# Optimization experiments

Measured on AMD Instinct MI355X. Metric: run time of the kernel, lower is better.

## Reference

```python
import jax, jax.numpy as jnp
import numpy as np


def _aggregate(x, w, k, pad):
    """Involution-style per-pixel local conv.
    x: [N, C, H, W]; w: [N, heads, wc, k*k, H, W] (stride=1, dilation=1, zero pad).
    Returns [N, heads, C, H, W].
    """
    N, C, H, W = x.shape
    heads, wc = w.shape[1], w.shape[2]
    G = C // wc  # channel groups sharing the same per-pixel weights (c % wc)
    xp = jnp.pad(x, ((0, 0), (0, 0), (pad, pad), (pad, pad)))
    # unfold: [N, C, k*k, H, W] via k*k static shifted slices (no dynamic indexing)
    patches = jnp.stack(
        [xp[:, :, i:i + H, j:j + W] for i in range(k) for j in range(k)], axis=2
    )
    p = patches.reshape(N, G, wc, k * k, H, W)
    # out[n, e, g, v, h, w] = sum_k w[n, e, v, k, h, w] * p[n, g, v, k, h, w]
    out = jnp.einsum('nevkhw,ngvkhw->negvhw', w, p)
    return out.reshape(N, heads, C, H, W)


def reference(x, weight1, weight2):
    out1 = _aggregate(x, weight1, 3, 1)  # 3x3 branch, pad=1
    out2 = _aggregate(x, weight2, 5, 2)  # 5x5 branch, pad=2
    # output layout [N, 2, heads, C, H, W] matching the CUDA index arithmetic
    return jnp.stack([out1, out2], axis=1)


def setup_inputs() -> dict:
    key = jax.random.key(0)
    k1, k2, k3 = jax.random.split(key, 3)
    N, C, H, W = 4, 256, 56, 56
    heads, wc = 1, 32
    x = jax.random.normal(k1, (N, C, H, W), dtype=jnp.float32)
    weight1 = jax.random.normal(k2, (N, heads, wc, 9, H, W), dtype=jnp.float32)
    weight2 = jax.random.normal(k3, (N, heads, wc, 25, H, W), dtype=jnp.float32)
    return {"x": x, "weight1": weight1, "weight2": weight2}
```

## Files before the change

### kernel.cpp

```cpp
#include <hip/hip_runtime.h>


#define N_  4
#define C_  256
#define H_  56
#define W_  56
#define HW_ 3136
#define WC_ 32
#define G_  8
#define W2_ 28
#define HW2_ 1568

__global__ __launch_bounds__(256) void lconv_kernel(
    const float* __restrict__ x,
    const float* __restrict__ w1,
    const float* __restrict__ w2,
    float* __restrict__ out)
{
    const int gid = blockIdx.x * 256 + threadIdx.x;
    const int hw2 = gid % HW2_;
    const int nv  = gid / HW2_;
    const int v   = nv % WC_;
    const int n   = nv / WC_;
    const int h   = hw2 / W2_;
    const int wb  = (hw2 % W2_) * 2;
    const int hw  = h * W_ + wb;

    const float* w1t = w1 + (size_t)nv * 9  * HW_ + hw;
    const float* w2t = w2 + (size_t)nv * 25 * HW_ + hw;
    const float* xb  = x + ((size_t)n * C_ + v) * HW_ + hw;

    float acc1x[G_], acc1y[G_], acc2x[G_], acc2y[G_];
    #pragma unroll
    for (int g = 0; g < G_; ++g) { acc1x[g]=0.f; acc1y[g]=0.f; acc2x[g]=0.f; acc2y[g]=0.f; }

    const bool aok = (wb > 0);
    const bool cok = (wb < W_ - 2);

    #pragma unroll
    for (int di = 0; di < 5; ++di) {
        const int hh = h + di - 2;
        const bool hok = (hh >= 0) && (hh < H_);

        float2 wr2[5];
        #pragma unroll
        for (int dj = 0; dj < 5; ++dj)
            wr2[dj] = *(const float2*)(w2t + (size_t)(di * 5 + dj) * HW_);
        float2 wr1[3];
        if (di >= 1 && di <= 3) {
            #pragma unroll
            for (int dj = 0; dj < 3; ++dj)
                wr1[dj] = *(const float2*)(w1t + (size_t)((di - 1) * 3 + dj) * HW_);
        }

        const int rowoff = (di - 2) * W_;
        #pragma unroll
        for (int g = 0; g < G_; ++g) {
            const float* xr = xb + (size_t)g * WC_ * HW_ + rowoff;
            const float2 z = make_float2(0.f, 0.f);
            float2 xa = (hok && aok) ? *(const float2*)(xr - 2) : z;
            float2 xm =  hok         ? *(const float2*)(xr)     : z;
            float2 xc = (hok && cok) ? *(const float2*)(xr + 2) : z;
            const float xw[6] = {xa.x, xa.y, xm.x, xm.y, xc.x, xc.y};

            #pragma unroll
            for (int dj = 0; dj < 5; ++dj) {
                acc2x[g] += wr2[dj].x * xw[dj];
                acc2y[g] += wr2[dj].y * xw[dj + 1];
            }
            if (di >= 1 && di <= 3) {
                #pragma unroll
                for (int dj = 0; dj < 3; ++dj) {
                    acc1x[g] += wr1[dj].x * xw[dj + 1];
                    acc1y[g] += wr1[dj].y * xw[dj + 2];
                }
            }
        }
    }

    float* o1 = out + ((size_t)(n * 2 + 0) * C_ + v) * HW_ + hw;
    float* o2 = out + ((size_t)(n * 2 + 1) * C_ + v) * HW_ + hw;
    #pragma unroll
    for (int g = 0; g < G_; ++g) {
        *(float2*)(o1 + (size_t)g * WC_ * HW_) = make_float2(acc1x[g], acc1y[g]);
        *(float2*)(o2 + (size_t)g * WC_ * HW_) = make_float2(acc2x[g], acc2y[g]);
    }
}

extern "C" void kernel_launch(void* const* d_in, const int* in_sizes, int n_in,
                              void* d_out, int out_size, void* d_ws, size_t ws_size,
                              hipStream_t stream) {
    const float* x  = (const float*)d_in[0];
    const float* w1 = (const float*)d_in[1];
    const float* w2 = (const float*)d_in[2];
    float* out = (float*)d_out;

    const int total = N_ * WC_ * HW2_;
    dim3 grid(total / 256), block(256);
    hipLaunchKernelGGL(lconv_kernel, grid, block, 0, stream, x, w1, w2, out);
}
```

Baseline: 135.6 us.

## Split channel groups across threads and widen pixel tile to four

Each thread now computes 4 adjacent output pixels for 2 of the 8 channel groups instead of 2 pixels for all 8 groups, using float4 loads and stores. This cuts per-thread register use and multiplies thread count to raise occupancy and latency hiding. The trade-off is that per-pixel weights are now loaded by four different threads, one per group pair, increasing weight traffic that must be served from cache.

```diff
diff --git a/kernel.cpp b/kernel.cpp
--- a/kernel.cpp
+++ b/kernel.cpp
@@ -1,89 +1,102 @@
 #include <hip/hip_runtime.h>
 
 
-#define N_  4
-#define C_  256
-#define H_  56
-#define W_  56
-#define HW_ 3136
-#define WC_ 32
-#define G_  8
-#define W2_ 28
-#define HW2_ 1568
+#define N_   4
+#define C_   256
+#define H_   56
+#define W_   56
+#define HW_  3136
+#define WC_  32
+#define W4_  14
+#define HW4_ 784
 
-__global__ __launch_bounds__(256) void lconv_kernel(
+__global__ __launch_bounds__(256, 4) void lconv_kernel(
     const float* __restrict__ x,
     const float* __restrict__ w1,
     const float* __restrict__ w2,
     float* __restrict__ out)
 {
-    const int gid = blockIdx.x * 256 + threadIdx.x;
-    const int hw2 = gid % HW2_;
-    const int nv  = gid / HW2_;
-    const int v   = nv % WC_;
-    const int n   = nv / WC_;
-    const int h   = hw2 / W2_;
-    const int wb  = (hw2 % W2_) * 2;
-    const int hw  = h * W_ + wb;
+    const int gid  = blockIdx.x * 256 + threadIdx.x;
+    const int hw4  = gid % HW4_;
+    const int rest = gid / HW4_;
+    const int gh   = rest % 4;
+    const int v    = (rest / 4) % WC_;
+    const int n    = rest / (4 * WC_);
+    const int h    = hw4 / W4_;
+    const int w4   = (hw4 % W4_) * 4;
+    const int hw   = h * W_ + w4;
+    const int nv   = n * WC_ + v;
 
     const float* w1t = w1 + (size_t)nv * 9  * HW_ + hw;
     const float* w2t = w2 + (size_t)nv * 25 * HW_ + hw;
-    const float* xb  = x + ((size_t)n * C_ + v) * HW_ + hw;
+    const int c0 = (2 * gh) * WC_ + v;
+    const float* xb = x + ((size_t)n * C_ + c0) * HW_ + hw;
 
-    float acc1x[G_], acc1y[G_], acc2x[G_], acc2y[G_];
+    float a1[2][4], a2[2][4];
     #pragma unroll
-    for (int g = 0; g < G_; ++g) { acc1x[g]=0.f; acc1y[g]=0.f; acc2x[g]=0.f; acc2y[g]=0.f; }
+    for (int g = 0; g < 2; ++g)
+        #pragma unroll
+        for (int p = 0; p < 4; ++p) { a1[g][p] = 0.f; a2[g][p] = 0.f; }
 
-    const bool aok = (wb > 0);
-    const bool cok = (wb < W_ - 2);
+    const bool aok = (w4 > 0);
+    const bool cok = (w4 < W_ - 4);
 
     #pragma unroll
     for (int di = 0; di < 5; ++di) {
         const int hh = h + di - 2;
         const bool hok = (hh >= 0) && (hh < H_);
+        const bool inner = (di >= 1) && (di <= 3);
 
-        float2 wr2[5];
+        float wr2[5][4];
         #pragma unroll
-        for (int dj = 0; dj < 5; ++dj)
-            wr2[dj] = *(const float2*)(w2t + (size_t)(di * 5 + dj) * HW_);
-        float2 wr1[3];
-        if (di >= 1 && di <= 3) {
+        for (int dj = 0; dj < 5; ++dj) {
+            const float4 t = *(const float4*)(w2t + (size_t)(di * 5 + dj) * HW_);
+            wr2[dj][0] = t.x; wr2[dj][1] = t.y; wr2[dj][2] = t.z; wr2[dj][3] = t.w;
+        }
+        float wr1[3][4];
+        if (inner) {
             #pragma unroll
-            for (int dj = 0; dj < 3; ++dj)
-                wr1[dj] = *(const float2*)(w1t + (size_t)((di - 1) * 3 + dj) * HW_);
+            for (int dj = 0; dj < 3; ++dj) {
+                const float4 t = *(const float4*)(w1t + (size_t)((di - 1) * 3 + dj) * HW_);
+                wr1[dj][0] = t.x; wr1[dj][1] = t.y; wr1[dj][2] = t.z; wr1[dj][3] = t.w;
+            }
         }
 
         const int rowoff = (di - 2) * W_;
         #pragma unroll
-        for (int g = 0; g < G_; ++g) {
+        for (int g = 0; g < 2; ++g) {
             const float* xr = xb + (size_t)g * WC_ * HW_ + rowoff;
-            const float2 z = make_float2(0.f, 0.f);
-            float2 xa = (hok && aok) ? *(const float2*)(xr - 2) : z;
-            float2 xm =  hok         ? *(const float2*)(xr)     : z;
-            float2 xc = (hok && cok) ? *(const float2*)(xr + 2) : z;
-            const float xw[6] = {xa.x, xa.y, xm.x, xm.y, xc.x, xc.y};
+            const float4 z = make_float4(0.f, 0.f, 0.f, 0.f);
+            const float4 xa = (hok && aok) ? *(const float4*)(xr - 4) : z;
+            const float4 xm =  hok         ? *(const float4*)(xr)     : z;
+            const float4 xc = (hok && cok) ? *(const float4*)(xr + 4) : z;
+            const float xw[12] = {xa.x, xa.y, xa.z, xa.w,
+                                  xm.x, xm.y, xm.z, xm.w,
+                                  xc.x, xc.y, xc.z, xc.w};
 
             #pragma unroll
-            for (int dj = 0; dj < 5; ++dj) {
-                acc2x[g] += wr2[dj].x * xw[dj];
-                acc2y[g] += wr2[dj].y * xw[dj + 1];
-            }
-            if (di >= 1 && di <= 3) {
+            for (int dj = 0; dj < 5; ++dj)
                 #pragma unroll
-                for (int dj = 0; dj < 3; ++dj) {
-                    acc1x[g] += wr1[dj].x * xw[dj + 1];
-                    acc1y[g] += wr1[dj].y * xw[dj + 2];
-                }
+                for (int p = 0; p < 4; ++p)
+                    a2[g][p] += wr2[dj][p] * xw[p + dj + 2];
+            if (inner) {
+                #pragma unroll
+                for (int dj = 0; dj < 3; ++dj)
+                    #pragma unroll
+                    for (int p = 0; p < 4; ++p)
+                        a1[g][p] += wr1[dj][p] * xw[p + dj + 3];
             }
         }
     }
 
-    float* o1 = out + ((size_t)(n * 2 + 0) * C_ + v) * HW_ + hw;
-    float* o2 = out + ((size_t)(n * 2 + 1) * C_ + v) * HW_ + hw;
+    float* o1 = out + ((size_t)(n * 2 + 0) * C_ + c0) * HW_ + hw;
+    float* o2 = out + ((size_t)(n * 2 + 1) * C_ + c0) * HW_ + hw;
     #pragma unroll
-    for (int g = 0; g < G_; ++g) {
-        *(float2*)(o1 + (size_t)g * WC_ * HW_) = make_float2(acc1x[g], acc1y[g]);
-        *(float2*)(o2 + (size_t)g * WC_ * HW_) = make_float2(acc2x[g], acc2y[g]);
+    for (int g = 0; g < 2; ++g) {
+        *(float4*)(o1 + (size_t)g * WC_ * HW_) =
+            make_float4(a1[g][0], a1[g][1], a1[g][2], a1[g][3]);
+        *(float4*)(o2 + (size_t)g * WC_ * HW_) =
+            make_float4(a2[g][0], a2[g][1], a2[g][2], a2[g][3]);
     }
 }
 
@@ -95,7 +108,7 @@
     const float* w2 = (const float*)d_in[2];
     float* out = (float*)d_out;
 
-    const int total = N_ * WC_ * HW2_;
+    const int total = N_ * WC_ * 4 * HW4_;
     dim3 grid(total / 256), block(256);
     hipLaunchKernelGGL(lconv_kernel, grid, block, 0, stream, x, w1, w2, out);
 }
```

After: 252.3 us. +86.1%, slower.

## Split channel groups across four threads to raise thread-level parallelism

Applied to the files above, without the earlier changes.

Each thread now computes 2 of the 8 channel groups instead of all 8, and the grid grows fourfold. Groups are interleaved into the low bits of the thread index, so four neighbouring lanes share the same per-pixel weights. The goal is higher occupancy and more latency hiding on a kernel that launched only a few blocks per CU. The trade-offs are redundant weight loads, x loads strided across channels within a wavefront, an un-unrolled di loop, and always-executed 3x3 FMAs on zeroed weights in the outer rows.

```diff
diff --git a/kernel.cpp b/kernel.cpp
--- a/kernel.cpp
+++ b/kernel.cpp
@@ -1,14 +1,13 @@
 #include <hip/hip_runtime.h>
 
 
-#define N_  4
-#define C_  256
-#define H_  56
-#define W_  56
-#define HW_ 3136
-#define WC_ 32
-#define G_  8
-#define W2_ 28
+#define N_   4
+#define C_   256
+#define H_   56
+#define W_   56
+#define HW_  3136
+#define WC_  32
+#define W2_  28
 #define HW2_ 1568
 
 __global__ __launch_bounds__(256) void lconv_kernel(
@@ -18,36 +17,42 @@
     float* __restrict__ out)
 {
     const int gid = blockIdx.x * 256 + threadIdx.x;
-    const int hw2 = gid % HW2_;
-    const int nv  = gid / HW2_;
-    const int v   = nv % WC_;
-    const int n   = nv / WC_;
+    const int gh  = gid & 3;
+    const int t   = gid >> 2;
+    const int hw2 = t % HW2_;
+    const int nv  = t / HW2_;
+    const int v   = nv & 31;
+    const int n   = nv >> 5;
     const int h   = hw2 / W2_;
     const int wb  = (hw2 % W2_) * 2;
     const int hw  = h * W_ + wb;
 
     const float* w1t = w1 + (size_t)nv * 9  * HW_ + hw;
     const float* w2t = w2 + (size_t)nv * 25 * HW_ + hw;
-    const float* xb  = x + ((size_t)n * C_ + v) * HW_ + hw;
+    const int c0 = gh * 64 + v;
+    const float* xb = x + ((size_t)n * C_ + c0) * HW_ + hw;
 
-    float acc1x[G_], acc1y[G_], acc2x[G_], acc2y[G_];
-    #pragma unroll
-    for (int g = 0; g < G_; ++g) { acc1x[g]=0.f; acc1y[g]=0.f; acc2x[g]=0.f; acc2y[g]=0.f; }
+    float a1x[2] = {0.f, 0.f}, a1y[2] = {0.f, 0.f};
+    float a2x[2] = {0.f, 0.f}, a2y[2] = {0.f, 0.f};
 
     const bool aok = (wb > 0);
     const bool cok = (wb < W_ - 2);
 
-    #pragma unroll
+    #pragma unroll 1
     for (int di = 0; di < 5; ++di) {
         const int hh = h + di - 2;
         const bool hok = (hh >= 0) && (hh < H_);
+        const bool inner = (di >= 1) && (di <= 3);
 
         float2 wr2[5];
         #pragma unroll
         for (int dj = 0; dj < 5; ++dj)
             wr2[dj] = *(const float2*)(w2t + (size_t)(di * 5 + dj) * HW_);
         float2 wr1[3];
-        if (di >= 1 && di <= 3) {
+        #pragma unroll
+        for (int dj = 0; dj < 3; ++dj)
+            wr1[dj] = make_float2(0.f, 0.f);
+        if (inner) {
             #pragma unroll
             for (int dj = 0; dj < 3; ++dj)
                 wr1[dj] = *(const float2*)(w1t + (size_t)((di - 1) * 3 + dj) * HW_);
@@ -55,35 +60,33 @@
 
         const int rowoff = (di - 2) * W_;
         #pragma unroll
-        for (int g = 0; g < G_; ++g) {
+        for (int g = 0; g < 2; ++g) {
             const float* xr = xb + (size_t)g * WC_ * HW_ + rowoff;
             const float2 z = make_float2(0.f, 0.f);
-            float2 xa = (hok && aok) ? *(const float2*)(xr - 2) : z;
-            float2 xm =  hok         ? *(const float2*)(xr)     : z;
-            float2 xc = (hok && cok) ? *(const float2*)(xr + 2) : z;
+            const float2 xa = (hok && aok) ? *(const float2*)(xr - 2) : z;
+            const float2 xm =  hok         ? *(const float2*)(xr)     : z;
+            const float2 xc = (hok && cok) ? *(const float2*)(xr + 2) : z;
             const float xw[6] = {xa.x, xa.y, xm.x, xm.y, xc.x, xc.y};
 
             #pragma unroll
             for (int dj = 0; dj < 5; ++dj) {
-                acc2x[g] += wr2[dj].x * xw[dj];
-                acc2y[g] += wr2[dj].y * xw[dj + 1];
+                a2x[g] += wr2[dj].x * xw[dj];
+                a2y[g] += wr2[dj].y * xw[dj + 1];
             }
-            if (di >= 1 && di <= 3) {
-                #pragma unroll
-                for (int dj = 0; dj < 3; ++dj) {
-                    acc1x[g] += wr1[dj].x * xw[dj + 1];
-                    acc1y[g] += wr1[dj].y * xw[dj + 2];
-                }
+            #pragma unroll
+            for (int dj = 0; dj < 3; ++dj) {
+                a1x[g] += wr1[dj].x * xw[dj + 1];
+                a1y[g] += wr1[dj].y * xw[dj + 2];
             }
         }
     }
 
-    float* o1 = out + ((size_t)(n * 2 + 0) * C_ + v) * HW_ + hw;
-    float* o2 = out + ((size_t)(n * 2 + 1) * C_ + v) * HW_ + hw;
+    float* o1 = out + ((size_t)(n * 2 + 0) * C_ + c0) * HW_ + hw;
+    float* o2 = out + ((size_t)(n * 2 + 1) * C_ + c0) * HW_ + hw;
     #pragma unroll
-    for (int g = 0; g < G_; ++g) {
-        *(float2*)(o1 + (size_t)g * WC_ * HW_) = make_float2(acc1x[g], acc1y[g]);
-        *(float2*)(o2 + (size_t)g * WC_ * HW_) = make_float2(acc2x[g], acc2y[g]);
+    for (int g = 0; g < 2; ++g) {
+        *(float2*)(o1 + (size_t)g * WC_ * HW_) = make_float2(a1x[g], a1y[g]);
+        *(float2*)(o2 + (size_t)g * WC_ * HW_) = make_float2(a2x[g], a2y[g]);
     }
 }
 
@@ -95,7 +98,7 @@
     const float* w2 = (const float*)d_in[2];
     float* out = (float*)d_out;
 
-    const int total = N_ * WC_ * HW2_;
+    const int total = N_ * WC_ * HW2_ * 4;
     dim3 grid(total / 256), block(256);
     hipLaunchKernelGGL(lconv_kernel, grid, block, 0, stream, x, w1, w2, out);
 }
```

Result: slower. 139.8 us (+3.2%).

## Stage input row tiles in LDS and split channel groups across blocks

Applied to the files above, without the earlier changes.

Each block now covers an 8-row spatial tile for one (n, v) and half of the channel groups. It cooperatively loads 12 padded input rows for 4 channel planes into shared memory, with zeroed halo columns, and computes from there, which removes the per-thread boundary-checked global loads of x. Because each block handles only 4 channel groups instead of 8, the per-pixel weights w1 and w2 are read from global memory twice as often. Some threads (cp >= 28) sit idle after the load phase, and the di loop is no longer unrolled.

```diff
diff --git a/kernel.cpp b/kernel.cpp
--- a/kernel.cpp
+++ b/kernel.cpp
@@ -7,9 +7,9 @@
 #define W_  56
 #define HW_ 3136
 #define WC_ 32
-#define G_  8
-#define W2_ 28
-#define HW2_ 1568
+
+#define LROWS   12
+#define LSTRIDE 64
 
 __global__ __launch_bounds__(256) void lconv_kernel(
     const float* __restrict__ x,
@@ -17,73 +17,102 @@
     const float* __restrict__ w2,
     float* __restrict__ out)
 {
-    const int gid = blockIdx.x * 256 + threadIdx.x;
-    const int hw2 = gid % HW2_;
-    const int nv  = gid / HW2_;
-    const int v   = nv % WC_;
-    const int n   = nv / WC_;
-    const int h   = hw2 / W2_;
-    const int wb  = (hw2 % W2_) * 2;
-    const int hw  = h * W_ + wb;
+    __shared__ float lds[4 * LROWS * LSTRIDE];
+
+    const int b    = blockIdx.x;
+    const int tile = b % 7;
+    const int gsel = (b / 7) & 1;
+    const int v    = (b / 14) & 31;
+    const int n    = b / 448;
+    const int r0   = tile * 8;
+    const int nv   = n * WC_ + v;
+    const int tid  = threadIdx.x;
+
+    for (int idx = tid; idx < 672; idx += 256) {
+        const int c4 = idx % 14;
+        const int t2 = idx / 14;
+        const int lr = t2 % LROWS;
+        const int pl = t2 / LROWS;
+        const int gr = r0 - 2 + lr;
+        float4 val = make_float4(0.f, 0.f, 0.f, 0.f);
+        if (gr >= 0 && gr < H_) {
+            const int ch = gsel * 128 + pl * 32 + v;
+            val = *(const float4*)(x + (size_t)(n * C_ + ch) * HW_ + gr * W_ + c4 * 4);
+        }
+        *(float4*)&lds[(pl * LROWS + lr) * LSTRIDE + 4 + c4 * 4] = val;
+    }
+    if (tid < 192) {
+        const int pl = tid / 48;
+        const int lr = (tid % 48) / 4;
+        const int k  = tid & 3;
+        const int slot = (k < 2) ? (2 + k) : (58 + k);
+        lds[(pl * LROWS + lr) * LSTRIDE + slot] = 0.f;
+    }
+    __syncthreads();
+
+    const int row = tid >> 5;
+    const int cp  = tid & 31;
+    if (cp >= 28) return;
+
+    const int h  = r0 + row;
+    const int wb = cp * 2;
+    const int hw = h * W_ + wb;
 
     const float* w1t = w1 + (size_t)nv * 9  * HW_ + hw;
     const float* w2t = w2 + (size_t)nv * 25 * HW_ + hw;
-    const float* xb  = x + ((size_t)n * C_ + v) * HW_ + hw;
 
-    float acc1x[G_], acc1y[G_], acc2x[G_], acc2y[G_];
-    #pragma unroll
-    for (int g = 0; g < G_; ++g) { acc1x[g]=0.f; acc1y[g]=0.f; acc2x[g]=0.f; acc2y[g]=0.f; }
+    float a1x[4] = {0.f,0.f,0.f,0.f}, a1y[4] = {0.f,0.f,0.f,0.f};
+    float a2x[4] = {0.f,0.f,0.f,0.f}, a2y[4] = {0.f,0.f,0.f,0.f};
 
-    const bool aok = (wb > 0);
-    const bool cok = (wb < W_ - 2);
-
-    #pragma unroll
+    #pragma unroll 1
     for (int di = 0; di < 5; ++di) {
-        const int hh = h + di - 2;
-        const bool hok = (hh >= 0) && (hh < H_);
+        const bool inner = (di >= 1) && (di <= 3);
 
         float2 wr2[5];
         #pragma unroll
         for (int dj = 0; dj < 5; ++dj)
             wr2[dj] = *(const float2*)(w2t + (size_t)(di * 5 + dj) * HW_);
-        float2 wr1[3];
-        if (di >= 1 && di <= 3) {
+        float2 wr1[3] = {make_float2(0.f,0.f), make_float2(0.f,0.f), make_float2(0.f,0.f)};
+        if (inner) {
             #pragma unroll
             for (int dj = 0; dj < 3; ++dj)
                 wr1[dj] = *(const float2*)(w1t + (size_t)((di - 1) * 3 + dj) * HW_);
         }
 
-        const int rowoff = (di - 2) * W_;
+        float2 xwa[4], xwb[4], xwc[4];
         #pragma unroll
-        for (int g = 0; g < G_; ++g) {
-            const float* xr = xb + (size_t)g * WC_ * HW_ + rowoff;
-            const float2 z = make_float2(0.f, 0.f);
-            float2 xa = (hok && aok) ? *(const float2*)(xr - 2) : z;
-            float2 xm =  hok         ? *(const float2*)(xr)     : z;
-            float2 xc = (hok && cok) ? *(const float2*)(xr + 2) : z;
-            const float xw[6] = {xa.x, xa.y, xm.x, xm.y, xc.x, xc.y};
+        for (int j = 0; j < 4; ++j) {
+            const float* lp = &lds[(j * LROWS + row + di) * LSTRIDE + wb + 2];
+            xwa[j] = *(const float2*)(lp);
+            xwb[j] = *(const float2*)(lp + 2);
+            xwc[j] = *(const float2*)(lp + 4);
+        }
 
+        #pragma unroll
+        for (int j = 0; j < 4; ++j) {
+            const float xw[6] = {xwa[j].x, xwa[j].y, xwb[j].x, xwb[j].y, xwc[j].x, xwc[j].y};
             #pragma unroll
             for (int dj = 0; dj < 5; ++dj) {
-                acc2x[g] += wr2[dj].x * xw[dj];
-                acc2y[g] += wr2[dj].y * xw[dj + 1];
+                a2x[j] += wr2[dj].x * xw[dj];
+                a2y[j] += wr2[dj].y * xw[dj + 1];
             }
-            if (di >= 1 && di <= 3) {
+            if (inner) {
                 #pragma unroll
                 for (int dj = 0; dj < 3; ++dj) {
-                    acc1x[g] += wr1[dj].x * xw[dj + 1];
-                    acc1y[g] += wr1[dj].y * xw[dj + 2];
+                    a1x[j] += wr1[dj].x * xw[dj + 1];
+                    a1y[j] += wr1[dj].y * xw[dj + 2];
                 }
             }
         }
     }
 
-    float* o1 = out + ((size_t)(n * 2 + 0) * C_ + v) * HW_ + hw;
-    float* o2 = out + ((size_t)(n * 2 + 1) * C_ + v) * HW_ + hw;
+    const int c0 = gsel * 128 + v;
+    float* o1 = out + ((size_t)(n * 2 + 0) * C_ + c0) * HW_ + hw;
+    float* o2 = out + ((size_t)(n * 2 + 1) * C_ + c0) * HW_ + hw;
     #pragma unroll
-    for (int g = 0; g < G_; ++g) {
-        *(float2*)(o1 + (size_t)g * WC_ * HW_) = make_float2(acc1x[g], acc1y[g]);
-        *(float2*)(o2 + (size_t)g * WC_ * HW_) = make_float2(acc2x[g], acc2y[g]);
+    for (int j = 0; j < 4; ++j) {
+        *(float2*)(o1 + (size_t)j * WC_ * HW_) = make_float2(a1x[j], a1y[j]);
+        *(float2*)(o2 + (size_t)j * WC_ * HW_) = make_float2(a2x[j], a2y[j]);
     }
 }
 
@@ -95,7 +124,6 @@
     const float* w2 = (const float*)d_in[2];
     float* out = (float*)d_out;
 
-    const int total = N_ * WC_ * HW2_;
-    dim3 grid(total / 256), block(256);
+    dim3 grid(4 * 32 * 2 * 7), block(256);
     hipLaunchKernelGGL(lconv_kernel, grid, block, 0, stream, x, w1, w2, out);
 }
```

Measured after the change: 112.8 us. -16.8%, faster.
